# Kernel optimization log

Measured on AMD Instinct MI355X. Metric: run time of the kernel, lower is better.

Reference implementation:

```python
import jax, jax.numpy as jnp
import numpy as np

NEG = -9e15  # matches -9000000000000000.0 in the torch source


def setup_inputs() -> dict:
    key = jax.random.key(0)
    k1, k2, k3, k4 = jax.random.split(key, 4)
    N, F_in, F_out = 8192, 512, 64
    h = jax.random.normal(k1, (N, F_in), dtype=jnp.float32)
    adj = jax.random.randint(k2, (N, N), 0, 2, dtype=jnp.int32)
    # xavier_uniform with gain=1.414
    def xavier(k, shape, gain=1.414):
        fan_in, fan_out = shape[0], shape[1]
        bound = gain * np.sqrt(6.0 / (fan_in + fan_out))
        return jax.random.uniform(k, shape, dtype=jnp.float32, minval=-bound, maxval=bound)
    W = xavier(k3, (F_in, F_out))
    a = xavier(k4, (2 * F_out, 1))
    return {"h": h, "adj": adj, "W": W, "a": a}


def reference(h, adj, W, a):
    alpha = 0.2
    F_out = W.shape[1]
    Wh = h.astype(jnp.float32) @ W                      # [N, F_out]
    # e[i,j] = leakyrelu( Wh[i] . a[:F_out] + Wh[j] . a[F_out:] )
    Wh1 = Wh @ a[:F_out, :]                             # [N, 1]
    Wh2 = Wh @ a[F_out:, :]                             # [N, 1]
    e = jax.nn.leaky_relu(Wh1 + Wh2.T, negative_slope=alpha)  # [N, N]
    scores = jnp.where(adj > 0, e, NEG)                 # mask non-edges
    attention = jax.nn.softmax(scores, axis=1)          # row softmax
    h_prime = attention @ Wh                            # [N, F_out]
    return h_prime
```

## Files before the change

### kernel.cpp

```cpp
#include <hip/hip_runtime.h>
#include <cstdint>
#include <cstddef>


#define GAT_N    8192
#define GAT_FIN  512
#define GAT_F    64
#define TJ       64
#define JSPLIT   4
#define JCHUNK   (GAT_N / JSPLIT)
#define NTILES   (JCHUNK / TJ)

typedef __attribute__((ext_vector_type(8))) short short8;
typedef __attribute__((ext_vector_type(4))) float f32x4;

__device__ __forceinline__ float lrelu(float x) { return fmaxf(x, 0.2f * x); }

__device__ __forceinline__ unsigned enc_f32(float f) {
    unsigned b = __float_as_uint(f);
    return b ^ ((b & 0x80000000u) ? 0xFFFFFFFFu : 0x80000000u);
}
__device__ __forceinline__ float dec_f32(unsigned u) {
    return __uint_as_float(u ^ ((u & 0x80000000u) ? 0x80000000u : 0xFFFFFFFFu));
}
__device__ __forceinline__ short f2bf_trunc(float f) {
    return (short)(__float_as_uint(f) >> 16);
}
__device__ __forceinline__ float bfhi(float f) {
    return __uint_as_float(__float_as_uint(f) & 0xFFFF0000u);
}

__device__ __forceinline__ void gload_lds16(const void* g, void* l) {
    __builtin_amdgcn_global_load_lds(
        (const __attribute__((address_space(1))) void*)g,
        (__attribute__((address_space(3))) void*)l, 16, 0, 0);
}

__global__ __launch_bounds__(256) void k_wh(
    const float* __restrict__ h, const float* __restrict__ W,
    const float* __restrict__ a,
    float* __restrict__ wh1, float* __restrict__ wh2,
    unsigned int* __restrict__ mw2,
    unsigned short* __restrict__ whtHi, unsigned short* __restrict__ whtLo)
{
    __shared__ float sW[2][64 * GAT_F];
    __shared__ unsigned short sTh[GAT_F][16];
    __shared__ unsigned short sTl[GAT_F][16];
    __shared__ unsigned int smax[16];
    const int tid = threadIdx.x;
    const size_t r0 = (size_t)blockIdx.x * 16;
    const int rp = tid >> 4;
    const int f4 = (tid & 15) * 4;

    const char* wsrc = (const char*)W;
    {
        char* dst = (char*)sW[0];
#pragma unroll
        for (int c = 0; c < 4; ++c)
            gload_lds16(wsrc + (size_t)(tid + c * 256) * 16,
                        dst + (size_t)(tid + c * 256) * 16);
    }

    const float* ha = h + (r0 + rp) * GAT_FIN;
    float4 acc = {0.f, 0.f, 0.f, 0.f};

    for (int ck = 0; ck < 8; ++ck) {
        __syncthreads();
        if (ck + 1 < 8) {
            const char* src = wsrc + (size_t)(ck + 1) * 16384;
            char* dst = (char*)sW[(ck + 1) & 1];
#pragma unroll
            for (int c = 0; c < 4; ++c)
                gload_lds16(src + (size_t)(tid + c * 256) * 16,
                            dst + (size_t)(tid + c * 256) * 16);
        }
        const float* wcp = sW[ck & 1];
#pragma unroll 4
        for (int k4 = 0; k4 < 16; ++k4) {
            float4 hv = *(const float4*)&ha[ck * 64 + k4 * 4];
            const float* hvf = (const float*)&hv;
#pragma unroll
            for (int kk = 0; kk < 4; ++kk) {
                float4 wv = *(const float4*)&wcp[(k4 * 4 + kk) * GAT_F + f4];
                acc.x = fmaf(hvf[kk], wv.x, acc.x);
                acc.y = fmaf(hvf[kk], wv.y, acc.y);
                acc.z = fmaf(hvf[kk], wv.z, acc.z);
                acc.w = fmaf(hvf[kk], wv.w, acc.w);
            }
        }
    }

    float4 a1 = *(const float4*)&a[f4];
    float4 a2 = *(const float4*)&a[GAT_F + f4];
    float pa = acc.x*a1.x + acc.y*a1.y + acc.z*a1.z + acc.w*a1.w;
    float pb = acc.x*a2.x + acc.y*a2.y + acc.z*a2.z + acc.w*a2.w;
#pragma unroll
    for (int m = 1; m < 16; m <<= 1) {
        pa += __shfl_xor(pa, m);
        pb += __shfl_xor(pb, m);
    }
    if ((tid & 15) == 0) {
        wh1[r0 + rp] = pa;
        wh2[r0 + rp] = pb;
        smax[rp] = enc_f32(pb);
    }

    const float* af = (const float*)&acc;
#pragma unroll
    for (int e = 0; e < 4; ++e) {
        float v = af[e];
        sTh[f4 + e][rp] = (unsigned short)f2bf_trunc(v);
        sTl[f4 + e][rp] = (unsigned short)f2bf_trunc(v - bfhi(v));
    }
    __syncthreads();

    {
        const int f = tid >> 2, rq = tid & 3;
        uint2 vh = *(const uint2*)&sTh[f][rq * 4];
        uint2 vl = *(const uint2*)&sTl[f][rq * 4];
        *(uint2*)&whtHi[(size_t)f * GAT_N + r0 + rq * 4] = vh;
        *(uint2*)&whtLo[(size_t)f * GAT_N + r0 + rq * 4] = vl;
    }
    if (tid == 0) {
        unsigned m = smax[0];
#pragma unroll
        for (int r = 1; r < 16; ++r) m = max(m, smax[r]);
        atomicMax(mw2, m);
    }
}

__global__ __launch_bounds__(256, 3) void k_attend(
    const int* __restrict__ adj,
    const unsigned short* __restrict__ whtHi,
    const unsigned short* __restrict__ whtLo,
    const float* __restrict__ wh1, const float* __restrict__ wh2,
    const unsigned int* __restrict__ mw2,
    float* __restrict__ po, float* __restrict__ pl)
{
    __shared__ char sB[2][16384];

    const int tid  = threadIdx.x;
    const int w    = tid >> 6;
    const int lane = tid & 63;
    const int fl   = lane & 15;
    const int jg   = lane >> 4;
    const int rw   = blockIdx.x * 64 + w * 16;
    const int j0   = blockIdx.y * JCHUNK;

    const float Mw2 = dec_f32(*mw2);
    const float ai  = wh1[rw + fl];
    const float Mi  = lrelu(ai + Mw2);

    const char* ssrc[4]; int sdst[4];
#pragma unroll
    for (int c = 0; c < 4; ++c) {
        int G = tid + (c & 1) * 256;
        int f = G >> 3, g = G & 7;
        const unsigned short* base = (c < 2) ? whtHi : whtLo;
        ssrc[c] = (const char*)(base + (size_t)f * GAT_N + j0 + ((g ^ (f & 7)) * 8));
        sdst[c] = ((c < 2) ? 0 : 8192) + G * 16;
    }

    const int off0 = fl * 128 + (((0 * 4 + jg) ^ (fl & 7)) * 16);
    const int off1 = fl * 128 + (((1 * 4 + jg) ^ (fl & 7)) * 16);

    const int*   ap = adj + (size_t)(rw + fl) * GAT_N + j0 + jg * 8;
    const float* wp = wh2 + j0 + jg * 8;

    {
#pragma unroll
        for (int c = 0; c < 4; ++c)
            gload_lds16(ssrc[c], (char*)sB[0] + sdst[c]);
    }
    int4 ac[4]; float4 wc[4];
#pragma unroll
    for (int q = 0; q < 4; ++q) {
        int o = (q >> 1) * 32 + (q & 1) * 4;
        ac[q] = *(const int4*)(ap + o);
        wc[q] = *(const float4*)(wp + o);
    }

    f32x4 acc[4] = {};
    float psum = 0.f;

    for (int t = 0; t < NTILES; ++t) {
        const int cur = t & 1;
        __syncthreads();

        if (t + 1 < NTILES) {
#pragma unroll
            for (int c = 0; c < 4; ++c)
                gload_lds16(ssrc[c] + (size_t)(t + 1) * 128,
                            (char*)sB[cur ^ 1] + sdst[c]);
        }
        const int tn = (t + 1 < NTILES) ? t + 1 : t;
        int4 an[4]; float4 wn[4];
#pragma unroll
        for (int q = 0; q < 4; ++q) {
            int o = tn * TJ + (q >> 1) * 32 + (q & 1) * 4;
            an[q] = *(const int4*)(ap + o);
            wn[q] = *(const float4*)(wp + o);
        }

        const char* sbc = sB[cur];
#pragma unroll
        for (int s = 0; s < 2; ++s) {
            float pv[8];
#pragma unroll
            for (int hh = 0; hh < 2; ++hh) {
                const int*   avi = (const int*)&ac[s * 2 + hh];
                const float* bvf = (const float*)&wc[s * 2 + hh];
#pragma unroll
                for (int e = 0; e < 4; ++e) {
                    float sc = lrelu(ai + bvf[e]);
                    float pe = __expf(sc - Mi);
                    pv[hh * 4 + e] = (avi[e] > 0) ? pe : 0.f;
                }
            }
            short8 ph, plo;
#pragma unroll
            for (int e = 0; e < 8; ++e) {
                psum  += pv[e];
                ph[e]  = f2bf_trunc(pv[e]);
                plo[e] = f2bf_trunc(pv[e] - bfhi(pv[e]));
            }
            const int offs = s ? off1 : off0;
#pragma unroll
            for (int nb = 0; nb < 4; ++nb) {
                short8 bh = *(const short8*)(sbc + offs + nb * 2048);
                short8 bl = *(const short8*)(sbc + 8192 + offs + nb * 2048);
                acc[nb] = __builtin_amdgcn_mfma_f32_16x16x32_bf16(ph,  bh, acc[nb], 0, 0, 0);
                acc[nb] = __builtin_amdgcn_mfma_f32_16x16x32_bf16(plo, bh, acc[nb], 0, 0, 0);
                acc[nb] = __builtin_amdgcn_mfma_f32_16x16x32_bf16(ph,  bl, acc[nb], 0, 0, 0);
            }
        }
#pragma unroll
        for (int q = 0; q < 4; ++q) { ac[q] = an[q]; wc[q] = wn[q]; }
    }

    psum += __shfl_xor(psum, 16);
    psum += __shfl_xor(psum, 32);
    if (lane < 16)
        pl[(size_t)blockIdx.y * GAT_N + rw + lane] = psum;

    const size_t ob = ((size_t)blockIdx.y * GAT_N + rw + jg * 4) * GAT_F + fl;
#pragma unroll
    for (int nb = 0; nb < 4; ++nb) {
#pragma unroll
        for (int r = 0; r < 4; ++r)
            po[ob + (size_t)r * GAT_F + nb * 16] = acc[nb][r];
    }
}

__global__ __launch_bounds__(256) void k_merge(
    const float* __restrict__ po, const float* __restrict__ pl,
    float* __restrict__ out)
{
    const int idx = blockIdx.x * 256 + threadIdx.x;
    const int i = idx >> 6;
    float s = 0.f, ls = 0.f;
#pragma unroll
    for (int y = 0; y < JSPLIT; ++y) {
        s  += po[(size_t)y * GAT_N * GAT_F + idx];
        ls += pl[(size_t)y * GAT_N + i];
    }
    out[idx] = s / ls;
}

extern "C" void kernel_launch(void* const* d_in, const int* in_sizes, int n_in,
                              void* d_out, int out_size, void* d_ws, size_t ws_size,
                              hipStream_t stream) {
    (void)in_sizes; (void)n_in; (void)out_size; (void)ws_size;
    const float* h   = (const float*)d_in[0];
    const int*   adj = (const int*)d_in[1];
    const float* W   = (const float*)d_in[2];
    const float* a   = (const float*)d_in[3];
    float* out = (float*)d_out;

    char* wsb = (char*)d_ws;
    float*          wh1   = (float*)(wsb);
    float*          wh2   = (float*)(wsb + 32768);
    unsigned int*   mw2   = (unsigned int*)(wsb + 65536);
    unsigned short* whtHi = (unsigned short*)(wsb + 131072);
    unsigned short* whtLo = (unsigned short*)(wsb + 1179648);
    float*          po    = (float*)(wsb + 2228224);
    float*          pl    = (float*)(wsb + 10616832);

    hipMemsetAsync(mw2, 0, 4, stream);
    k_wh    <<<GAT_N / 16, 256, 0, stream>>>(h, W, a, wh1, wh2, mw2, whtHi, whtLo);
    k_attend<<<dim3(GAT_N / 64, JSPLIT), 256, 0, stream>>>(adj, whtHi, whtLo,
                                                           wh1, wh2, mw2, po, pl);
    k_merge <<<GAT_N * GAT_F / 256, 256, 0, stream>>>(po, pl, out);
}
```

Before: 427.4 us.

## Pre-pack adjacency into bitmask words and double the j-split

```diff
diff --git a/kernel.cpp b/kernel.cpp
--- a/kernel.cpp
+++ b/kernel.cpp
@@ -7,9 +7,10 @@
 #define GAT_FIN  512
 #define GAT_F    64
 #define TJ       64
-#define JSPLIT   4
+#define JSPLIT   8
 #define JCHUNK   (GAT_N / JSPLIT)
 #define NTILES   (JCHUNK / TJ)
+#define NWORDS   (GAT_N / 64)
 
 typedef __attribute__((ext_vector_type(8))) short short8;
 typedef __attribute__((ext_vector_type(4))) float f32x4;
@@ -34,6 +35,34 @@
     __builtin_amdgcn_global_load_lds(
         (const __attribute__((address_space(1))) void*)g,
         (__attribute__((address_space(3))) void*)l, 16, 0, 0);
+}
+
+__global__ __launch_bounds__(256) void k_pack(
+    const int* __restrict__ adj, unsigned long long* __restrict__ packed)
+{
+    const int lane = threadIdx.x & 63;
+    const int wv   = blockIdx.x * 4 + (threadIdx.x >> 6);
+    const size_t wbase = (size_t)wv * 256;
+    for (int it = 0; it < 32; ++it) {
+        const size_t w0 = wbase + (size_t)it * 8;
+        const int* src = adj + w0 * 64 + lane;
+        unsigned long long b0, b1, b2, b3, b4, b5, b6, b7;
+        b0 = __ballot(src[0 * 64] > 0);
+        b1 = __ballot(src[1 * 64] > 0);
+        b2 = __ballot(src[2 * 64] > 0);
+        b3 = __ballot(src[3 * 64] > 0);
+        b4 = __ballot(src[4 * 64] > 0);
+        b5 = __ballot(src[5 * 64] > 0);
+        b6 = __ballot(src[6 * 64] > 0);
+        b7 = __ballot(src[7 * 64] > 0);
+        if (lane == 0) {
+            ulonglong2* dst = (ulonglong2*)&packed[w0];
+            dst[0] = {b0, b1};
+            dst[1] = {b2, b3};
+            dst[2] = {b4, b5};
+            dst[3] = {b6, b7};
+        }
+    }
 }
 
 __global__ __launch_bounds__(256) void k_wh(
@@ -130,7 +159,7 @@
 }
 
 __global__ __launch_bounds__(256, 3) void k_attend(
-    const int* __restrict__ adj,
+    const unsigned long long* __restrict__ packed,
     const unsigned short* __restrict__ whtHi,
     const unsigned short* __restrict__ whtLo,
     const float* __restrict__ wh1, const float* __restrict__ wh2,
@@ -164,7 +193,7 @@
     const int off0 = fl * 128 + (((0 * 4 + jg) ^ (fl & 7)) * 16);
     const int off1 = fl * 128 + (((1 * 4 + jg) ^ (fl & 7)) * 16);
 
-    const int*   ap = adj + (size_t)(rw + fl) * GAT_N + j0 + jg * 8;
+    const unsigned long long* mp = packed + (size_t)(rw + fl) * NWORDS + (j0 >> 6);
     const float* wp = wh2 + j0 + jg * 8;
 
     {
@@ -172,13 +201,11 @@
         for (int c = 0; c < 4; ++c)
             gload_lds16(ssrc[c], (char*)sB[0] + sdst[c]);
     }
-    int4 ac[4]; float4 wc[4];
-#pragma unroll
-    for (int q = 0; q < 4; ++q) {
-        int o = (q >> 1) * 32 + (q & 1) * 4;
-        ac[q] = *(const int4*)(ap + o);
-        wc[q] = *(const float4*)(wp + o);
-    }
+    unsigned long long amc = mp[0];
+    float4 wc[4];
+#pragma unroll
+    for (int q = 0; q < 4; ++q)
+        wc[q] = *(const float4*)(wp + (q >> 1) * 32 + (q & 1) * 4);
 
     f32x4 acc[4] = {};
     float psum = 0.f;
@@ -194,27 +221,25 @@
                             (char*)sB[cur ^ 1] + sdst[c]);
         }
         const int tn = (t + 1 < NTILES) ? t + 1 : t;
-        int4 an[4]; float4 wn[4];
-#pragma unroll
-        for (int q = 0; q < 4; ++q) {
-            int o = tn * TJ + (q >> 1) * 32 + (q & 1) * 4;
-            an[q] = *(const int4*)(ap + o);
-            wn[q] = *(const float4*)(wp + o);
-        }
+        unsigned long long amn = mp[tn];
+        float4 wn[4];
+#pragma unroll
+        for (int q = 0; q < 4; ++q)
+            wn[q] = *(const float4*)(wp + tn * TJ + (q >> 1) * 32 + (q & 1) * 4);
 
         const char* sbc = sB[cur];
 #pragma unroll
         for (int s = 0; s < 2; ++s) {
+            const unsigned m8 = (unsigned)(amc >> (s * 32 + jg * 8)) & 0xFFu;
             float pv[8];
 #pragma unroll
             for (int hh = 0; hh < 2; ++hh) {
-                const int*   avi = (const int*)&ac[s * 2 + hh];
                 const float* bvf = (const float*)&wc[s * 2 + hh];
 #pragma unroll
                 for (int e = 0; e < 4; ++e) {
                     float sc = lrelu(ai + bvf[e]);
                     float pe = __expf(sc - Mi);
-                    pv[hh * 4 + e] = (avi[e] > 0) ? pe : 0.f;
+                    pv[hh * 4 + e] = ((m8 >> (hh * 4 + e)) & 1u) ? pe : 0.f;
                 }
             }
             short8 ph, plo;
@@ -234,8 +259,9 @@
                 acc[nb] = __builtin_amdgcn_mfma_f32_16x16x32_bf16(ph,  bl, acc[nb], 0, 0, 0);
             }
         }
-#pragma unroll
-        for (int q = 0; q < 4; ++q) { ac[q] = an[q]; wc[q] = wn[q]; }
+        amc = amn;
+#pragma unroll
+        for (int q = 0; q < 4; ++q) wc[q] = wn[q];
     }
 
     psum += __shfl_xor(psum, 16);
@@ -278,17 +304,19 @@
     float* out = (float*)d_out;
 
     char* wsb = (char*)d_ws;
-    float*          wh1   = (float*)(wsb);
-    float*          wh2   = (float*)(wsb + 32768);
-    unsigned int*   mw2   = (unsigned int*)(wsb + 65536);
-    unsigned short* whtHi = (unsigned short*)(wsb + 131072);
-    unsigned short* whtLo = (unsigned short*)(wsb + 1179648);
-    float*          po    = (float*)(wsb + 2228224);
-    float*          pl    = (float*)(wsb + 10616832);
+    float*              wh1    = (float*)(wsb);
+    float*              wh2    = (float*)(wsb + 32768);
+    unsigned int*       mw2    = (unsigned int*)(wsb + 65536);
+    unsigned long long* packed = (unsigned long long*)(wsb + 131072);
+    unsigned short*     whtHi  = (unsigned short*)(wsb + 8519680);
+    unsigned short*     whtLo  = (unsigned short*)(wsb + 9568256);
+    float*              po     = (float*)(wsb + 10616832);
+    float*              pl     = (float*)(wsb + 27394048);
 
     hipMemsetAsync(mw2, 0, 4, stream);
+    k_pack  <<<1024, 256, 0, stream>>>(adj, packed);
     k_wh    <<<GAT_N / 16, 256, 0, stream>>>(h, W, a, wh1, wh2, mw2, whtHi, whtLo);
-    k_attend<<<dim3(GAT_N / 64, JSPLIT), 256, 0, stream>>>(adj, whtHi, whtLo,
+    k_attend<<<dim3(GAT_N / 64, JSPLIT), 256, 0, stream>>>(packed, whtHi, whtLo,
                                                            wh1, wh2, mw2, po, pl);
     k_merge <<<GAT_N * GAT_F / 256, 256, 0, stream>>>(po, pl, out);
 }
```

Result: slower. 450.0 us (+5.3%).
